# Kernel optimization log

Measured on AMD Instinct MI355X. Metric: run time of the kernel, lower is better.

## Reference

```python
import jax, jax.numpy as jnp
import numpy as np

N = 8192
IN_DIM, HID_DIM, OUT_DIM = 32, 64, 16


def setup_inputs() -> dict:
    key = jax.random.key(0)
    k1, k2, k3, k4, k5, k6, k7 = jax.random.split(key, 7)
    s1 = 1.0 / np.sqrt(IN_DIM)
    s2 = 1.0 / np.sqrt(HID_DIM)
    return {
        "adj1": jax.random.normal(k1, (N, N), jnp.float32),
        "adj2": jax.random.normal(k2, (N, N), jnp.float32),
        "features": jax.random.normal(k3, (N, IN_DIM), jnp.float32),
        # gc1 linear (shared across both aggregation branches)
        "W1": jax.random.uniform(k4, (IN_DIM, HID_DIM), jnp.float32, -s1, s1),
        "b1": jax.random.uniform(k5, (HID_DIM,), jnp.float32, -s1, s1),
        # gc2 linear
        "W2": jax.random.uniform(k6, (HID_DIM, OUT_DIM), jnp.float32, -s2, s2),
        "b2": jax.random.uniform(k7, (OUT_DIM,), jnp.float32, -s2, s2),
    }


def _gc_layer(adj1, adj2, x, W, b):
    # branch 1: aggregate -> shared linear -> relu
    o1 = jax.nn.relu(jnp.matmul(adj1, x) @ W + b)
    # branch 2: same linear weights
    o2 = jax.nn.relu(jnp.matmul(adj2, x) @ W + b)
    return o1 + o2


def reference(adj1, adj2, features, W1, b1, W2, b2):
    h1 = _gc_layer(adj1, adj2, features, W1, b1)  # [N, HID_DIM]
    h2 = _gc_layer(adj1, adj2, h1, W2, b2)        # [N, OUT_DIM]
    return h2
```

## Files before the change

### kernel.cpp

```cpp
#include <hip/hip_runtime.h>
#include <stdint.h>

#define NN 8192
#define IN_DIM 32
#define HID_DIM 64
#define OUT_DIM 16

typedef __attribute__((ext_vector_type(8))) short short8;
typedef __attribute__((ext_vector_type(4))) float f32x4;

__device__ __forceinline__ short f2bf_bits(float x){
  uint32_t u = __builtin_bit_cast(uint32_t, x);
  u += 0x7FFFu + ((u >> 16) & 1u);
  return (short)(u >> 16);
}

__device__ __forceinline__ short8 cvt8(f32x4 lo, f32x4 hi){
  short8 r;
  r[0]=f2bf_bits(lo[0]); r[1]=f2bf_bits(lo[1]); r[2]=f2bf_bits(lo[2]); r[3]=f2bf_bits(lo[3]);
  r[4]=f2bf_bits(hi[0]); r[5]=f2bf_bits(hi[1]); r[6]=f2bf_bits(hi[2]); r[7]=f2bf_bits(hi[3]);
  return r;
}

__global__ __launch_bounds__(256) void prep_xt(const float* __restrict__ X, short* __restrict__ Xt){
  int i = blockIdx.x * 256 + threadIdx.x;
  int r = i >> 5, c = i & 31;
  Xt[(size_t)c * NN + r] = f2bf_bits(X[i]);
}

__global__ __launch_bounds__(256) void gcn_mm1(const float* __restrict__ adj1, const float* __restrict__ adj2,
                                               const short* __restrict__ Xt,
                                               float* __restrict__ Y1p, float* __restrict__ Y2p, int klen){
  const int lane = threadIdx.x & 63;
  const int wave = threadIdx.x >> 6;
  const int bm   = blockIdx.x;
  const int ks   = blockIdx.y;
  const int arow = bm * 64 + wave * 16 + (lane & 15);
  const int kgrp = (lane >> 4) * 8;
  const int k0   = ks * klen;

  const float* a1  = adj1 + (size_t)arow * NN + k0 + kgrp;
  const float* a2  = adj2 + (size_t)arow * NN + k0 + kgrp;
  const short* bp0 = Xt + (size_t)(lane & 15) * NN + k0 + kgrp;
  const short* bp1 = bp0 + (size_t)16 * NN;

  f32x4 acc10 = {0.f,0.f,0.f,0.f}, acc11 = {0.f,0.f,0.f,0.f};
  f32x4 acc20 = {0.f,0.f,0.f,0.f}, acc21 = {0.f,0.f,0.f,0.f};

  const int nsteps = klen >> 5;
  #pragma unroll 4
  for (int t = 0; t < nsteps; ++t){
    f32x4 a1lo = *(const f32x4*)(a1);
    f32x4 a1hi = *(const f32x4*)(a1 + 4);
    f32x4 a2lo = *(const f32x4*)(a2);
    f32x4 a2hi = *(const f32x4*)(a2 + 4);
    short8 b0  = *(const short8*)(bp0);
    short8 b1  = *(const short8*)(bp1);
    short8 fa1 = cvt8(a1lo, a1hi);
    short8 fa2 = cvt8(a2lo, a2hi);
    acc10 = __builtin_amdgcn_mfma_f32_16x16x32_bf16(fa1, b0, acc10, 0, 0, 0);
    acc11 = __builtin_amdgcn_mfma_f32_16x16x32_bf16(fa1, b1, acc11, 0, 0, 0);
    acc20 = __builtin_amdgcn_mfma_f32_16x16x32_bf16(fa2, b0, acc20, 0, 0, 0);
    acc21 = __builtin_amdgcn_mfma_f32_16x16x32_bf16(fa2, b1, acc21, 0, 0, 0);
    a1 += 32; a2 += 32; bp0 += 32; bp1 += 32;
  }

  const int orow = bm * 64 + wave * 16 + (lane >> 4) * 4;
  const int col  = lane & 15;
  float* y1 = Y1p + ((size_t)ks * NN + orow) * IN_DIM + col;
  float* y2 = Y2p + ((size_t)ks * NN + orow) * IN_DIM + col;
  #pragma unroll
  for (int r = 0; r < 4; ++r){
    y1[(size_t)r * IN_DIM]      = acc10[r];
    y1[(size_t)r * IN_DIM + 16] = acc11[r];
    y2[(size_t)r * IN_DIM]      = acc20[r];
    y2[(size_t)r * IN_DIM + 16] = acc21[r];
  }
}

__global__ __launch_bounds__(256) void l1_combine(const float* __restrict__ Y1p, const float* __restrict__ Y2p,
                                                  const float* __restrict__ W1, const float* __restrict__ b1,
                                                  short* __restrict__ H1t, int S){
  __shared__ float sW[IN_DIM * HID_DIM];
  __shared__ float sb[HID_DIM];
  __shared__ float sy[4][2][IN_DIM];
  const int tid = threadIdx.x;
  for (int i = tid; i < IN_DIM * HID_DIM; i += 256) sW[i] = W1[i];
  if (tid < HID_DIM) sb[tid] = b1[tid];
  const int sub = tid >> 6, t = tid & 63;
  const int row = blockIdx.x * 4 + sub;
  {
    const int br = t >> 5, c = t & 31;
    const float* P = br ? Y2p : Y1p;
    float s = 0.f;
    for (int sp = 0; sp < S; ++sp) s += P[((size_t)sp * NN + row) * IN_DIM + c];
    sy[sub][br][c] = s;
  }
  __syncthreads();
  float h1v = sb[t], h2v = sb[t];
  #pragma unroll
  for (int k = 0; k < IN_DIM; ++k){
    h1v += sy[sub][0][k] * sW[k * HID_DIM + t];
    h2v += sy[sub][1][k] * sW[k * HID_DIM + t];
  }
  float h = fmaxf(h1v, 0.f) + fmaxf(h2v, 0.f);
  H1t[(size_t)t * NN + row] = f2bf_bits(h);
}

__global__ __launch_bounds__(256) void gcn_mm2(const float* __restrict__ adj1, const float* __restrict__ adj2,
                                               const short* __restrict__ H1t,
                                               float* __restrict__ Z1p, float* __restrict__ Z2p, int klen){
  const int lane = threadIdx.x & 63;
  const int wave = threadIdx.x >> 6;
  const int bm   = blockIdx.x;
  const int ks   = blockIdx.y;
  const int arow = bm * 64 + wave * 16 + (lane & 15);
  const int kgrp = (lane >> 4) * 8;
  const int k0   = ks * klen;

  const float* a1 = adj1 + (size_t)arow * NN + k0 + kgrp;
  const float* a2 = adj2 + (size_t)arow * NN + k0 + kgrp;
  const short* bp[4];
  #pragma unroll
  for (int f = 0; f < 4; ++f)
    bp[f] = H1t + (size_t)(f * 16 + (lane & 15)) * NN + k0 + kgrp;

  f32x4 acc1[4] = {{0.f,0.f,0.f,0.f},{0.f,0.f,0.f,0.f},{0.f,0.f,0.f,0.f},{0.f,0.f,0.f,0.f}};
  f32x4 acc2[4] = {{0.f,0.f,0.f,0.f},{0.f,0.f,0.f,0.f},{0.f,0.f,0.f,0.f},{0.f,0.f,0.f,0.f}};

  const int nsteps = klen >> 5;
  #pragma unroll 2
  for (int t = 0; t < nsteps; ++t){
    f32x4 a1lo = *(const f32x4*)(a1);
    f32x4 a1hi = *(const f32x4*)(a1 + 4);
    f32x4 a2lo = *(const f32x4*)(a2);
    f32x4 a2hi = *(const f32x4*)(a2 + 4);
    short8 b[4];
    #pragma unroll
    for (int f = 0; f < 4; ++f) b[f] = *(const short8*)(bp[f]);
    short8 fa1 = cvt8(a1lo, a1hi);
    short8 fa2 = cvt8(a2lo, a2hi);
    #pragma unroll
    for (int f = 0; f < 4; ++f){
      acc1[f] = __builtin_amdgcn_mfma_f32_16x16x32_bf16(fa1, b[f], acc1[f], 0, 0, 0);
      acc2[f] = __builtin_amdgcn_mfma_f32_16x16x32_bf16(fa2, b[f], acc2[f], 0, 0, 0);
    }
    a1 += 32; a2 += 32;
    #pragma unroll
    for (int f = 0; f < 4; ++f) bp[f] += 32;
  }

  const int orow = bm * 64 + wave * 16 + (lane >> 4) * 4;
  const int col  = lane & 15;
  float* z1 = Z1p + ((size_t)ks * NN + orow) * HID_DIM + col;
  float* z2 = Z2p + ((size_t)ks * NN + orow) * HID_DIM + col;
  #pragma unroll
  for (int r = 0; r < 4; ++r){
    #pragma unroll
    for (int f = 0; f < 4; ++f){
      z1[(size_t)r * HID_DIM + f * 16] = acc1[f][r];
      z2[(size_t)r * HID_DIM + f * 16] = acc2[f][r];
    }
  }
}

__global__ __launch_bounds__(256) void l2_combine(const float* __restrict__ Z1p, const float* __restrict__ Z2p,
                                                  const float* __restrict__ W2, const float* __restrict__ b2,
                                                  float* __restrict__ out, int S){
  __shared__ float sW[HID_DIM * OUT_DIM];
  __shared__ float sb[OUT_DIM];
  __shared__ float sz[4][2][HID_DIM];
  const int tid = threadIdx.x;
  for (int i = tid; i < HID_DIM * OUT_DIM; i += 256) sW[i] = W2[i];
  if (tid < OUT_DIM) sb[tid] = b2[tid];
  const int sub = tid >> 6, t = tid & 63;
  const int row = blockIdx.x * 4 + sub;
  float s1 = 0.f, s2 = 0.f;
  for (int sp = 0; sp < S; ++sp){
    s1 += Z1p[((size_t)sp * NN + row) * HID_DIM + t];
    s2 += Z2p[((size_t)sp * NN + row) * HID_DIM + t];
  }
  sz[sub][0][t] = s1;
  sz[sub][1][t] = s2;
  __syncthreads();
  if (t < OUT_DIM){
    float a = sb[t], b = sb[t];
    #pragma unroll
    for (int k = 0; k < HID_DIM; ++k){
      a += sz[sub][0][k] * sW[k * OUT_DIM + t];
      b += sz[sub][1][k] * sW[k * OUT_DIM + t];
    }
    out[(size_t)row * OUT_DIM + t] = fmaxf(a, 0.f) + fmaxf(b, 0.f);
  }
}

extern "C" void kernel_launch(void* const* d_in, const int* in_sizes, int n_in,
                              void* d_out, int out_size, void* d_ws, size_t ws_size,
                              hipStream_t stream){
  const float* adj1 = (const float*)d_in[0];
  const float* adj2 = (const float*)d_in[1];
  const float* X    = (const float*)d_in[2];
  const float* W1   = (const float*)d_in[3];
  const float* b1   = (const float*)d_in[4];
  const float* W2   = (const float*)d_in[5];
  const float* b2   = (const float*)d_in[6];
  float* out = (float*)d_out;

  char* ws = (char*)d_ws;
  short* Xt  = (short*)ws;
  short* H1t = (short*)(ws + (size_t)512 * 1024);
  size_t off = (size_t)1536 * 1024;

  int S = 4;
  while (S > 1 && off + (size_t)S * 6 * 1024 * 1024 > ws_size) S >>= 1;
  float* Y1p = (float*)(ws + off);
  float* Y2p = Y1p + (size_t)S * NN * IN_DIM;
  float* Z1p = Y2p + (size_t)S * NN * IN_DIM;
  float* Z2p = Z1p + (size_t)S * NN * HID_DIM;
  const int klen = NN / S;

  prep_xt  <<<dim3(NN * IN_DIM / 256), dim3(256), 0, stream>>>(X, Xt);
  gcn_mm1  <<<dim3(NN / 64, S), dim3(256), 0, stream>>>(adj1, adj2, Xt, Y1p, Y2p, klen);
  l1_combine<<<dim3(NN / 4), dim3(256), 0, stream>>>(Y1p, Y2p, W1, b1, H1t, S);
  gcn_mm2  <<<dim3(NN / 64, S), dim3(256), 0, stream>>>(adj1, adj2, H1t, Z1p, Z2p, klen);
  l2_combine<<<dim3(NN / 4), dim3(256), 0, stream>>>(Z1p, Z2p, W2, b2, out, S);
}
```

Baseline: 267.0 us.

## Software-pipeline adjacency loads, reverse mm2 traversal for cache reuse, raise split-K

Both MFMA kernels now prefetch the next k-step's adjacency and feature fragments into registers while the current step converts and issues MFMAs. The loop unroll is dropped and launch bounds request 4 blocks per CU, aiming for better latency hiding. gcn_mm2 walks blocks and the k dimension in reverse order so the tail of adj1/adj2 left in L2/LLC by gcn_mm1 is reused first. Split-K S is raised from 4 to 8 for more parallelism, at the cost of larger partial buffers and more reduction work in the combine kernels.

```diff
diff --git a/kernel.cpp b/kernel.cpp
--- a/kernel.cpp
+++ b/kernel.cpp
@@ -28,9 +28,9 @@
   Xt[(size_t)c * NN + r] = f2bf_bits(X[i]);
 }
 
-__global__ __launch_bounds__(256) void gcn_mm1(const float* __restrict__ adj1, const float* __restrict__ adj2,
-                                               const short* __restrict__ Xt,
-                                               float* __restrict__ Y1p, float* __restrict__ Y2p, int klen){
+__global__ __launch_bounds__(256, 4) void gcn_mm1(const float* __restrict__ adj1, const float* __restrict__ adj2,
+                                                  const short* __restrict__ Xt,
+                                                  float* __restrict__ Y1p, float* __restrict__ Y2p, int klen){
   const int lane = threadIdx.x & 63;
   const int wave = threadIdx.x >> 6;
   const int bm   = blockIdx.x;
@@ -48,21 +48,32 @@
   f32x4 acc20 = {0.f,0.f,0.f,0.f}, acc21 = {0.f,0.f,0.f,0.f};
 
   const int nsteps = klen >> 5;
-  #pragma unroll 4
-  for (int t = 0; t < nsteps; ++t){
-    f32x4 a1lo = *(const f32x4*)(a1);
-    f32x4 a1hi = *(const f32x4*)(a1 + 4);
-    f32x4 a2lo = *(const f32x4*)(a2);
-    f32x4 a2hi = *(const f32x4*)(a2 + 4);
-    short8 b0  = *(const short8*)(bp0);
-    short8 b1  = *(const short8*)(bp1);
-    short8 fa1 = cvt8(a1lo, a1hi);
-    short8 fa2 = cvt8(a2lo, a2hi);
-    acc10 = __builtin_amdgcn_mfma_f32_16x16x32_bf16(fa1, b0, acc10, 0, 0, 0);
-    acc11 = __builtin_amdgcn_mfma_f32_16x16x32_bf16(fa1, b1, acc11, 0, 0, 0);
-    acc20 = __builtin_amdgcn_mfma_f32_16x16x32_bf16(fa2, b0, acc20, 0, 0, 0);
-    acc21 = __builtin_amdgcn_mfma_f32_16x16x32_bf16(fa2, b1, acc21, 0, 0, 0);
+
+  f32x4 A1l = *(const f32x4*)(a1), A1h = *(const f32x4*)(a1 + 4);
+  f32x4 A2l = *(const f32x4*)(a2), A2h = *(const f32x4*)(a2 + 4);
+  short8 B0 = *(const short8*)(bp0), B1 = *(const short8*)(bp1);
+
+  #pragma unroll 1
+  for (int t = 0; t < nsteps - 1; ++t){
     a1 += 32; a2 += 32; bp0 += 32; bp1 += 32;
+    f32x4 nA1l = *(const f32x4*)(a1), nA1h = *(const f32x4*)(a1 + 4);
+    f32x4 nA2l = *(const f32x4*)(a2), nA2h = *(const f32x4*)(a2 + 4);
+    short8 nB0 = *(const short8*)(bp0), nB1 = *(const short8*)(bp1);
+    short8 fa1 = cvt8(A1l, A1h);
+    short8 fa2 = cvt8(A2l, A2h);
+    acc10 = __builtin_amdgcn_mfma_f32_16x16x32_bf16(fa1, B0, acc10, 0, 0, 0);
+    acc11 = __builtin_amdgcn_mfma_f32_16x16x32_bf16(fa1, B1, acc11, 0, 0, 0);
+    acc20 = __builtin_amdgcn_mfma_f32_16x16x32_bf16(fa2, B0, acc20, 0, 0, 0);
+    acc21 = __builtin_amdgcn_mfma_f32_16x16x32_bf16(fa2, B1, acc21, 0, 0, 0);
+    A1l = nA1l; A1h = nA1h; A2l = nA2l; A2h = nA2h; B0 = nB0; B1 = nB1;
+  }
+  {
+    short8 fa1 = cvt8(A1l, A1h);
+    short8 fa2 = cvt8(A2l, A2h);
+    acc10 = __builtin_amdgcn_mfma_f32_16x16x32_bf16(fa1, B0, acc10, 0, 0, 0);
+    acc11 = __builtin_amdgcn_mfma_f32_16x16x32_bf16(fa1, B1, acc11, 0, 0, 0);
+    acc20 = __builtin_amdgcn_mfma_f32_16x16x32_bf16(fa2, B0, acc20, 0, 0, 0);
+    acc21 = __builtin_amdgcn_mfma_f32_16x16x32_bf16(fa2, B1, acc21, 0, 0, 0);
   }
 
   const int orow = bm * 64 + wave * 16 + (lane >> 4) * 4;
@@ -107,47 +118,63 @@
   H1t[(size_t)t * NN + row] = f2bf_bits(h);
 }
 
-__global__ __launch_bounds__(256) void gcn_mm2(const float* __restrict__ adj1, const float* __restrict__ adj2,
-                                               const short* __restrict__ H1t,
-                                               float* __restrict__ Z1p, float* __restrict__ Z2p, int klen){
+__global__ __launch_bounds__(256, 4) void gcn_mm2(const float* __restrict__ adj1, const float* __restrict__ adj2,
+                                                  const short* __restrict__ H1t,
+                                                  float* __restrict__ Z1p, float* __restrict__ Z2p, int klen){
   const int lane = threadIdx.x & 63;
   const int wave = threadIdx.x >> 6;
-  const int bm   = blockIdx.x;
-  const int ks   = blockIdx.y;
+  const int bm   = gridDim.x - 1 - blockIdx.x;
+  const int ks   = gridDim.y - 1 - blockIdx.y;
   const int arow = bm * 64 + wave * 16 + (lane & 15);
   const int kgrp = (lane >> 4) * 8;
-  const int k0   = ks * klen;
-
-  const float* a1 = adj1 + (size_t)arow * NN + k0 + kgrp;
-  const float* a2 = adj2 + (size_t)arow * NN + k0 + kgrp;
+  const int nsteps = klen >> 5;
+  const int klast  = ks * klen + (nsteps - 1) * 32;
+
+  const float* a1 = adj1 + (size_t)arow * NN + klast + kgrp;
+  const float* a2 = adj2 + (size_t)arow * NN + klast + kgrp;
   const short* bp[4];
   #pragma unroll
   for (int f = 0; f < 4; ++f)
-    bp[f] = H1t + (size_t)(f * 16 + (lane & 15)) * NN + k0 + kgrp;
+    bp[f] = H1t + (size_t)(f * 16 + (lane & 15)) * NN + klast + kgrp;
 
   f32x4 acc1[4] = {{0.f,0.f,0.f,0.f},{0.f,0.f,0.f,0.f},{0.f,0.f,0.f,0.f},{0.f,0.f,0.f,0.f}};
   f32x4 acc2[4] = {{0.f,0.f,0.f,0.f},{0.f,0.f,0.f,0.f},{0.f,0.f,0.f,0.f},{0.f,0.f,0.f,0.f}};
 
-  const int nsteps = klen >> 5;
-  #pragma unroll 2
-  for (int t = 0; t < nsteps; ++t){
-    f32x4 a1lo = *(const f32x4*)(a1);
-    f32x4 a1hi = *(const f32x4*)(a1 + 4);
-    f32x4 a2lo = *(const f32x4*)(a2);
-    f32x4 a2hi = *(const f32x4*)(a2 + 4);
-    short8 b[4];
-    #pragma unroll
-    for (int f = 0; f < 4; ++f) b[f] = *(const short8*)(bp[f]);
-    short8 fa1 = cvt8(a1lo, a1hi);
-    short8 fa2 = cvt8(a2lo, a2hi);
+  f32x4 A1l = *(const f32x4*)(a1), A1h = *(const f32x4*)(a1 + 4);
+  f32x4 A2l = *(const f32x4*)(a2), A2h = *(const f32x4*)(a2 + 4);
+  short8 B[4];
+  #pragma unroll
+  for (int f = 0; f < 4; ++f) B[f] = *(const short8*)(bp[f]);
+
+  #pragma unroll 1
+  for (int t = 0; t < nsteps - 1; ++t){
+    a1 -= 32; a2 -= 32;
+    #pragma unroll
+    for (int f = 0; f < 4; ++f) bp[f] -= 32;
+    f32x4 nA1l = *(const f32x4*)(a1), nA1h = *(const f32x4*)(a1 + 4);
+    f32x4 nA2l = *(const f32x4*)(a2), nA2h = *(const f32x4*)(a2 + 4);
+    short8 nB[4];
+    #pragma unroll
+    for (int f = 0; f < 4; ++f) nB[f] = *(const short8*)(bp[f]);
+    short8 fa1 = cvt8(A1l, A1h);
+    short8 fa2 = cvt8(A2l, A2h);
     #pragma unroll
     for (int f = 0; f < 4; ++f){
-      acc1[f] = __builtin_amdgcn_mfma_f32_16x16x32_bf16(fa1, b[f], acc1[f], 0, 0, 0);
-      acc2[f] = __builtin_amdgcn_mfma_f32_16x16x32_bf16(fa2, b[f], acc2[f], 0, 0, 0);
-    }
-    a1 += 32; a2 += 32;
-    #pragma unroll
-    for (int f = 0; f < 4; ++f) bp[f] += 32;
+      acc1[f] = __builtin_amdgcn_mfma_f32_16x16x32_bf16(fa1, B[f], acc1[f], 0, 0, 0);
+      acc2[f] = __builtin_amdgcn_mfma_f32_16x16x32_bf16(fa2, B[f], acc2[f], 0, 0, 0);
+    }
+    A1l = nA1l; A1h = nA1h; A2l = nA2l; A2h = nA2h;
+    #pragma unroll
+    for (int f = 0; f < 4; ++f) B[f] = nB[f];
+  }
+  {
+    short8 fa1 = cvt8(A1l, A1h);
+    short8 fa2 = cvt8(A2l, A2h);
+    #pragma unroll
+    for (int f = 0; f < 4; ++f){
+      acc1[f] = __builtin_amdgcn_mfma_f32_16x16x32_bf16(fa1, B[f], acc1[f], 0, 0, 0);
+      acc2[f] = __builtin_amdgcn_mfma_f32_16x16x32_bf16(fa2, B[f], acc2[f], 0, 0, 0);
+    }
   }
 
   const int orow = bm * 64 + wave * 16 + (lane >> 4) * 4;
@@ -211,7 +238,7 @@
   short* H1t = (short*)(ws + (size_t)512 * 1024);
   size_t off = (size_t)1536 * 1024;
 
-  int S = 4;
+  int S = 8;
   while (S > 1 && off + (size_t)S * 6 * 1024 * 1024 > ws_size) S >>= 1;
   float* Y1p = (float*)(ws + off);
   float* Y2p = Y1p + (size_t)S * NN * IN_DIM;
```

New measurement: 284.8 us. 6.7% more time.
